# Optimization experiments

Measured on AMD Instinct MI355X. Metric: run time of the kernel, lower is better.

Reference implementation:

```python
import jax, jax.numpy as jnp
import numpy as np

DIN = 128
HID = 128
B, N = 32, 2048
NEG = 9000000000000000.0


def setup_inputs() -> dict:
    key = jax.random.key(0)
    ks = jax.random.split(key, 8)
    x = jax.random.normal(ks[0], (B, N, DIN), dtype=jnp.float32)
    mask = jax.random.randint(ks[1], (B, N, N), 0, 2).astype(jnp.float32)
    s = 1.0 / np.sqrt(DIN)
    Wv = jax.random.uniform(ks[2], (DIN, HID), minval=-s, maxval=s, dtype=jnp.float32)
    bv = jax.random.uniform(ks[3], (HID,), minval=-s, maxval=s, dtype=jnp.float32)
    Wk = jax.random.uniform(ks[4], (DIN, HID), minval=-s, maxval=s, dtype=jnp.float32)
    bk = jax.random.uniform(ks[5], (HID,), minval=-s, maxval=s, dtype=jnp.float32)
    Wq = jax.random.uniform(ks[6], (DIN, HID), minval=-s, maxval=s, dtype=jnp.float32)
    bq = jax.random.uniform(ks[7], (HID,), minval=-s, maxval=s, dtype=jnp.float32)
    return {"x": x, "mask": mask, "Wv": Wv, "bv": bv, "Wk": Wk, "bk": bk, "Wq": Wq, "bq": bq}


def reference(x, mask, Wv, bv, Wk, bk, Wq, bq):
    v = jnp.tanh(x @ Wv + bv)            # [B, N, H]
    q = jnp.tanh(x @ Wq + bq)            # [B, N, H]
    k = jnp.tanh(x @ Wk + bk)            # [B, N, H]
    scores = jnp.einsum('bih,bjh->bij', q, k)  # [B, N, N]
    scores = scores * mask - NEG * (1.0 - mask)
    att = jax.nn.softmax(scores, axis=-1)
    out = jnp.einsum('bij,bjh->bih', att, v)   # [B, N, H]
    return out
```

## Files before the change

### kernel.cpp

```cpp
#include <hip/hip_runtime.h>

#define DIN 128
#define HID 128
#define BB  32
#define NN  2048
#define LOG2E 1.44269504088896340736f

typedef float  f32x4   __attribute__((ext_vector_type(4)));
typedef __bf16 bf16x4v __attribute__((ext_vector_type(4)));
typedef __bf16 bf16x8  __attribute__((ext_vector_type(8)));

__device__ __forceinline__ float tanh_fast(float x) {
  float e = __expf(2.0f * x);
  return 1.0f - 2.0f / (e + 1.0f);
}

__global__ __launch_bounds__(256) void wt_kernel(
    const float* __restrict__ Wq, const float* __restrict__ Wk,
    const float* __restrict__ Wv, __bf16* __restrict__ wt) {
  const float* W = (blockIdx.x == 0) ? Wq : (blockIdx.x == 1) ? Wk : Wv;
  __bf16* dst = wt + blockIdx.x * (DIN * HID);
  int t = threadIdx.x;
#pragma unroll
  for (int c = 0; c < 16; ++c) {
    int o = c * 1024 + t * 4;
    int d = o >> 7, h = o & 127;
    f32x4 v = *(const f32x4*)(W + d * HID + h);
    dst[(h + 0) * DIN + d] = (__bf16)v.x;
    dst[(h + 1) * DIN + d] = (__bf16)v.y;
    dst[(h + 2) * DIN + d] = (__bf16)v.z;
    dst[(h + 3) * DIN + d] = (__bf16)v.w;
  }
}

__global__ __launch_bounds__(256) void proj_kernel(
    const float* __restrict__ x, const __bf16* __restrict__ wt,
    const float* __restrict__ bq, const float* __restrict__ bk,
    const float* __restrict__ bv, __bf16* __restrict__ qbf,
    __bf16* __restrict__ kbf, __bf16* __restrict__ vtbf) {
  int tid = threadIdx.x;
  int lane = tid & 63, w = tid >> 6;
  int l15 = lane & 15, quad = lane >> 4;
  long i0 = (long)blockIdx.x * 64;

  bf16x8 bx[4][4];
#pragma unroll
  for (int nt = 0; nt < 4; ++nt) {
    const float* xp = x + (i0 + nt * 16 + l15) * DIN;
#pragma unroll
    for (int ks = 0; ks < 4; ++ks) {
      int d0 = ks * 32 + quad * 8;
      f32x4 a = *(const f32x4*)(xp + d0);
      f32x4 b = *(const f32x4*)(xp + d0 + 4);
      bf16x8 f;
      f[0] = (__bf16)a.x; f[1] = (__bf16)a.y; f[2] = (__bf16)a.z; f[3] = (__bf16)a.w;
      f[4] = (__bf16)b.x; f[5] = (__bf16)b.y; f[6] = (__bf16)b.z; f[7] = (__bf16)b.w;
      bx[nt][ks] = f;
    }
  }

#pragma unroll
  for (int p = 0; p < 2; ++p) {
    const __bf16* wtp = wt + p * DIN * HID;
    const float* bias = (p == 0) ? bq : bk;
    __bf16* outp = (p == 0) ? qbf : kbf;
#pragma unroll
    for (int nt = 0; nt < 8; ++nt) {
      int h0 = nt * 16 + l15;
      f32x4 acc = {0.f, 0.f, 0.f, 0.f};
#pragma unroll
      for (int ks = 0; ks < 4; ++ks) {
        bf16x8 wf = *(const bf16x8*)(wtp + (long)h0 * DIN + ks * 32 + quad * 8);
        acc = __builtin_amdgcn_mfma_f32_16x16x32_bf16(bx[w][ks], wf, acc, 0, 0, 0);
      }
      float bcol = bias[h0];
      long rowb = i0 + w * 16 + quad * 4;
#pragma unroll
      for (int r = 0; r < 4; ++r) {
        float val = tanh_fast(acc[r] + bcol);
        if (p == 0) val *= LOG2E;
        outp[(rowb + r) * HID + h0] = (__bf16)val;
      }
    }
  }

  {
    const __bf16* wtp = wt + 2 * DIN * HID;
    long bb = i0 >> 11;
    int nloc = (int)(i0 & 2047);
    long vbase = bb * (long)HID * NN;
#pragma unroll
    for (int s = 0; s < 2; ++s) {
      int hb = w * 32 + s * 16;
      bf16x8 af[4];
#pragma unroll
      for (int ks = 0; ks < 4; ++ks)
        af[ks] = *(const bf16x8*)(wtp + (long)(hb + l15) * DIN + ks * 32 + quad * 8);
      float bvr[4];
#pragma unroll
      for (int r = 0; r < 4; ++r) bvr[r] = bv[hb + quad * 4 + r];
#pragma unroll
      for (int nt = 0; nt < 4; ++nt) {
        f32x4 acc = {0.f, 0.f, 0.f, 0.f};
#pragma unroll
        for (int ks = 0; ks < 4; ++ks)
          acc = __builtin_amdgcn_mfma_f32_16x16x32_bf16(af[ks], bx[nt][ks], acc, 0, 0, 0);
        int hrow = hb + quad * 4;
        int ncol = nloc + nt * 16 + l15;
#pragma unroll
        for (int r = 0; r < 4; ++r) {
          float val = tanh_fast(acc[r] + bvr[r]);
          vtbf[vbase + (long)(hrow + r) * NN + ncol] = (__bf16)val;
        }
      }
    }
  }
}

__global__ __launch_bounds__(512, 4) void attn_kernel(
    const __bf16* __restrict__ qbf, const __bf16* __restrict__ kbf,
    const __bf16* __restrict__ vtbf, const float* __restrict__ mask,
    float* __restrict__ out) {
  __shared__ __bf16 Ks[2][64 * 128];
  __shared__ __bf16 Vts[2][128 * 64];

  const int tid = threadIdx.x;
  const int lane = tid & 63, w = tid >> 6;
  const int l15 = lane & 15, quad = lane >> 4;
  const int swz = (l15 & 7) << 3;
  const int bid = blockIdx.x;
  const int vb = (bid >> 3) | ((bid & 7) << 6);
  const int b = vb >> 4;
  const int i0 = (vb & 15) * 128;
  const long kvbase = (long)b * NN * HID;

  bf16x8 qf[4];
  {
    const __bf16* qp = qbf + kvbase + (long)(i0 + w * 16 + l15) * HID + quad * 8;
#pragma unroll
    for (int ks = 0; ks < 4; ++ks) qf[ks] = *(const bf16x8*)(qp + ks * 32);
  }

  const int krl = (w << 3) + (lane >> 3);
  const int kcl = (lane & 7) * 8;
  const int vrl = (w << 4) + (lane >> 2);
  const int vcl = (lane & 3) * 8;
  const __bf16* kg = kbf + kvbase + (long)krl * HID + kcl;
  const __bf16* vg = vtbf + (long)b * HID * NN + (long)vrl * NN + vcl;
  const int ksw0 = krl * 128 + (kcl ^ ((krl & 7) << 3));
  const int ksw1 = krl * 128 + ((kcl + 64) ^ ((krl & 7) << 3));
  const int vsw0 = vrl * 64 + (vcl ^ ((vrl & 7) << 3));
  const int vsw1 = vrl * 64 + ((vcl + 32) ^ ((vrl & 7) << 3));
  const float* mp = mask + ((long)b * NN + (i0 + w * 16 + l15)) * NN + quad * 4;

  f32x4 O[8];
#pragma unroll
  for (int i = 0; i < 8; ++i) O[i] = (f32x4){0.f, 0.f, 0.f, 0.f};
  float mrow = -1e30f, lrow = 0.0f;

  bf16x8 kr0 = *(const bf16x8*)(kg);
  bf16x8 kr1 = *(const bf16x8*)(kg + 64);
  bf16x8 vr0 = *(const bf16x8*)(vg);
  bf16x8 vr1 = *(const bf16x8*)(vg + 32);
  f32x4 mr[4];
#pragma unroll
  for (int t = 0; t < 4; ++t) mr[t] = *(const f32x4*)(mp + t * 16);
  *(bf16x8*)&Ks[0][ksw0] = kr0; *(bf16x8*)&Ks[0][ksw1] = kr1;
  *(bf16x8*)&Vts[0][vsw0] = vr0; *(bf16x8*)&Vts[0][vsw1] = vr1;
  unsigned mbits;
  {
    float mb = 0.f;
#pragma unroll
    for (int t = 0; t < 4; ++t)
#pragma unroll
      for (int r = 0; r < 4; ++r)
        mb = fmaf(mr[t][r], (float)(1u << (t * 4 + r)), mb);
    mbits = (unsigned)mb;
  }
  __syncthreads();

  int cur = 0;
  for (int jt = 0; jt < 32; ++jt) {
    const int jn = (jt < 31) ? jt + 1 : 31;
    {
      const __bf16* kgn = kg + (long)jn * 64 * HID;
      kr0 = *(const bf16x8*)(kgn);
      kr1 = *(const bf16x8*)(kgn + 64);
      const __bf16* vgn = vg + jn * 64;
      vr0 = *(const bf16x8*)(vgn);
      vr1 = *(const bf16x8*)(vgn + 32);
#pragma unroll
      for (int t = 0; t < 4; ++t) mr[t] = *(const f32x4*)(mp + jn * 64 + t * 16);
    }

    f32x4 pt[4];
#pragma unroll
    for (int t = 0; t < 4; ++t) {
      f32x4 acc = {0.f, 0.f, 0.f, 0.f};
      const int krow = t * 16 + l15;
#pragma unroll
      for (int ks = 0; ks < 4; ++ks) {
        bf16x8 kf = *(const bf16x8*)&Ks[cur][krow * 128 + ((quad * 8 + ks * 32) ^ swz)];
        acc = __builtin_amdgcn_mfma_f32_16x16x32_bf16(kf, qf[ks], acc, 0, 0, 0);
      }
      pt[t] = acc;
    }

    float tmx = -1e30f;
#pragma unroll
    for (int t = 0; t < 4; ++t)
#pragma unroll
      for (int r = 0; r < 4; ++r) {
        float s = ((mbits >> (t * 4 + r)) & 1u) ? pt[t][r] : -1e30f;
        pt[t][r] = s;
        tmx = fmaxf(tmx, s);
      }
    tmx = fmaxf(tmx, __shfl_xor(tmx, 16));
    tmx = fmaxf(tmx, __shfl_xor(tmx, 32));
    const bool grow = !__all(tmx <= mrow);
    const float mnew = fmaxf(mrow, tmx);
    const float alpha = exp2f(mrow - mnew);
    float rs = 0.0f;
#pragma unroll
    for (int t = 0; t < 4; ++t)
#pragma unroll
      for (int r = 0; r < 4; ++r) {
        float p = exp2f(pt[t][r] - mnew);
        pt[t][r] = p;
        rs += p;
      }
    rs += __shfl_xor(rs, 16);
    rs += __shfl_xor(rs, 32);
    lrow = lrow * alpha + rs;
    mrow = mnew;

    if (grow) {
      float ar[4];
#pragma unroll
      for (int r = 0; r < 4; ++r) ar[r] = __shfl(alpha, (quad << 2) + r);
#pragma unroll
      for (int nt = 0; nt < 8; ++nt)
#pragma unroll
        for (int r = 0; r < 4; ++r) O[nt][r] *= ar[r];
    }

    __bf16* Pw = &Ks[cur ^ 1][w * 1024];
#pragma unroll
    for (int t = 0; t < 4; ++t) {
      bf16x4v pb;
#pragma unroll
      for (int r = 0; r < 4; ++r) pb[r] = (__bf16)pt[t][r];
      *(bf16x4v*)&Pw[l15 * 64 + ((t * 16 + quad * 4) ^ swz)] = pb;
    }
    const bf16x8 pf0 = *(const bf16x8*)&Pw[l15 * 64 + ((quad * 8) ^ swz)];
    const bf16x8 pf1 = *(const bf16x8*)&Pw[l15 * 64 + ((quad * 8 + 32) ^ swz)];

#pragma unroll
    for (int nt = 0; nt < 8; ++nt) {
      const int vrow = nt * 16 + l15;
      bf16x8 vf0 = *(const bf16x8*)&Vts[cur][vrow * 64 + ((quad * 8) ^ swz)];
      bf16x8 vf1 = *(const bf16x8*)&Vts[cur][vrow * 64 + ((quad * 8 + 32) ^ swz)];
      O[nt] = __builtin_amdgcn_mfma_f32_16x16x32_bf16(pf0, vf0, O[nt], 0, 0, 0);
      O[nt] = __builtin_amdgcn_mfma_f32_16x16x32_bf16(pf1, vf1, O[nt], 0, 0, 0);
    }

    *(bf16x8*)&Ks[cur ^ 1][ksw0] = kr0; *(bf16x8*)&Ks[cur ^ 1][ksw1] = kr1;
    *(bf16x8*)&Vts[cur ^ 1][vsw0] = vr0; *(bf16x8*)&Vts[cur ^ 1][vsw1] = vr1;
    {
      float mb = 0.f;
#pragma unroll
      for (int t = 0; t < 4; ++t)
#pragma unroll
        for (int r = 0; r < 4; ++r)
          mb = fmaf(mr[t][r], (float)(1u << (t * 4 + r)), mb);
      mbits = (unsigned)mb;
    }
    __syncthreads();
    cur ^= 1;
  }

  const float inv = 1.0f / lrow;
  float il[4];
#pragma unroll
  for (int r = 0; r < 4; ++r) il[r] = __shfl(inv, (quad << 2) + r);
  const long rowb = (long)b * NN + i0 + w * 16 + quad * 4;
#pragma unroll
  for (int r = 0; r < 4; ++r) {
    float* op = out + (rowb + r) * HID;
#pragma unroll
    for (int nt = 0; nt < 8; ++nt) op[nt * 16 + l15] = O[nt][r] * il[r];
  }
}

extern "C" void kernel_launch(void* const* d_in, const int* in_sizes, int n_in,
                              void* d_out, int out_size, void* d_ws, size_t ws_size,
                              hipStream_t stream) {
  const float* x    = (const float*)d_in[0];
  const float* mask = (const float*)d_in[1];
  const float* Wv   = (const float*)d_in[2];
  const float* bv   = (const float*)d_in[3];
  const float* Wk   = (const float*)d_in[4];
  const float* bk   = (const float*)d_in[5];
  const float* Wq   = (const float*)d_in[6];
  const float* bq   = (const float*)d_in[7];
  float* out = (float*)d_out;

  __bf16* ws = (__bf16*)d_ws;
  __bf16* wt   = ws;
  __bf16* qbf  = ws + 3 * DIN * HID;
  __bf16* kbf  = qbf + (long)BB * NN * HID;
  __bf16* vtbf = kbf + (long)BB * NN * HID;

  wt_kernel<<<3, 256, 0, stream>>>(Wq, Wk, Wv, wt);
  proj_kernel<<<BB * NN / 64, 256, 0, stream>>>(x, wt, bq, bk, bv, qbf, kbf, vtbf);
  attn_kernel<<<512, 512, 0, stream>>>(qbf, kbf, vtbf, mask, out);
}
```

Before: 893.3 us.

## Switch attention kernel to 32x32x16 MFMA with register-resident P and 4 waves

Rewrites the attention kernel to use 32x32x16 bf16 MFMAs, with each wave owning 32 query rows instead of 16 and blocks shrinking to 256 threads. Probabilities are passed to the PV MFMA through cross-half lane shuffles instead of a round trip through shared memory. The output store becomes row-contiguous float4 writes. The aim is fewer MFMA issues, fewer LDS accesses and a cheaper output store, in exchange for more accumulator registers per thread and fewer waves per block.

```diff
diff --git a/kernel.cpp b/kernel.cpp
--- a/kernel.cpp
+++ b/kernel.cpp
@@ -7,12 +7,19 @@
 #define LOG2E 1.44269504088896340736f
 
 typedef float  f32x4   __attribute__((ext_vector_type(4)));
+typedef float  f32x16  __attribute__((ext_vector_type(16)));
 typedef __bf16 bf16x4v __attribute__((ext_vector_type(4)));
 typedef __bf16 bf16x8  __attribute__((ext_vector_type(8)));
 
 __device__ __forceinline__ float tanh_fast(float x) {
   float e = __expf(2.0f * x);
   return 1.0f - 2.0f / (e + 1.0f);
+}
+
+__device__ __forceinline__ unsigned pack2bf(float x, float y) {
+  union { unsigned u; __bf16 h[2]; } t;
+  t.h[0] = (__bf16)x; t.h[1] = (__bf16)y;
+  return t.u;
 }
 
 __global__ __launch_bounds__(256) void wt_kernel(
@@ -117,7 +124,7 @@
   }
 }
 
-__global__ __launch_bounds__(512, 4) void attn_kernel(
+__global__ __launch_bounds__(256, 2) void attn_kernel(
     const __bf16* __restrict__ qbf, const __bf16* __restrict__ kbf,
     const __bf16* __restrict__ vtbf, const float* __restrict__ mask,
     float* __restrict__ out) {
@@ -126,56 +133,62 @@
 
   const int tid = threadIdx.x;
   const int lane = tid & 63, w = tid >> 6;
-  const int l15 = lane & 15, quad = lane >> 4;
-  const int swz = (l15 & 7) << 3;
+  const int l31 = lane & 31, H = lane >> 5;
+  const int swz = (l31 & 7) << 3;
   const int bid = blockIdx.x;
   const int vb = (bid >> 3) | ((bid & 7) << 6);
   const int b = vb >> 4;
   const int i0 = (vb & 15) * 128;
   const long kvbase = (long)b * NN * HID;
-
-  bf16x8 qf[4];
+  const int qrow = i0 + w * 32 + l31;
+
+  bf16x8 qf[8];
   {
-    const __bf16* qp = qbf + kvbase + (long)(i0 + w * 16 + l15) * HID + quad * 8;
-#pragma unroll
-    for (int ks = 0; ks < 4; ++ks) qf[ks] = *(const bf16x8*)(qp + ks * 32);
-  }
-
-  const int krl = (w << 3) + (lane >> 3);
-  const int kcl = (lane & 7) * 8;
-  const int vrl = (w << 4) + (lane >> 2);
-  const int vcl = (lane & 3) * 8;
-  const __bf16* kg = kbf + kvbase + (long)krl * HID + kcl;
-  const __bf16* vg = vtbf + (long)b * HID * NN + (long)vrl * NN + vcl;
-  const int ksw0 = krl * 128 + (kcl ^ ((krl & 7) << 3));
-  const int ksw1 = krl * 128 + ((kcl + 64) ^ ((krl & 7) << 3));
-  const int vsw0 = vrl * 64 + (vcl ^ ((vrl & 7) << 3));
-  const int vsw1 = vrl * 64 + ((vcl + 32) ^ ((vrl & 7) << 3));
-  const float* mp = mask + ((long)b * NN + (i0 + w * 16 + l15)) * NN + quad * 4;
-
-  f32x4 O[8];
-#pragma unroll
-  for (int i = 0; i < 8; ++i) O[i] = (f32x4){0.f, 0.f, 0.f, 0.f};
+    const __bf16* qp = qbf + kvbase + (long)qrow * HID + H * 8;
+#pragma unroll
+    for (int kd = 0; kd < 8; ++kd) qf[kd] = *(const bf16x8*)(qp + kd * 16);
+  }
+
+  const __bf16* kg = kbf + kvbase + (long)tid * 8;
+  const int ksw = (tid >> 4) * 128 + (((tid & 15) * 8) ^ (((tid >> 4) & 7) << 3));
+  const int vrow = tid >> 1, vcolb = (tid & 1) * 32;
+  const __bf16* vg = vtbf + (long)b * HID * NN + (long)vrow * NN + vcolb;
+  int vsw[4];
+#pragma unroll
+  for (int u = 0; u < 4; ++u)
+    vsw[u] = vrow * 64 + ((vcolb + u * 8) ^ ((vrow & 7) << 3));
+  const float* mp = mask + ((long)b * NN + qrow) * NN + H * 4;
+
+  f32x16 O[4];
+#pragma unroll
+  for (int ht = 0; ht < 4; ++ht)
+#pragma unroll
+    for (int r = 0; r < 16; ++r) O[ht][r] = 0.f;
   float mrow = -1e30f, lrow = 0.0f;
 
-  bf16x8 kr0 = *(const bf16x8*)(kg);
-  bf16x8 kr1 = *(const bf16x8*)(kg + 64);
-  bf16x8 vr0 = *(const bf16x8*)(vg);
-  bf16x8 vr1 = *(const bf16x8*)(vg + 32);
-  f32x4 mr[4];
-#pragma unroll
-  for (int t = 0; t < 4; ++t) mr[t] = *(const f32x4*)(mp + t * 16);
-  *(bf16x8*)&Ks[0][ksw0] = kr0; *(bf16x8*)&Ks[0][ksw1] = kr1;
-  *(bf16x8*)&Vts[0][vsw0] = vr0; *(bf16x8*)&Vts[0][vsw1] = vr1;
+  bf16x8 kr[4], vr[4];
+  f32x4 mr[8];
+#pragma unroll
+  for (int u = 0; u < 4; ++u) kr[u] = *(const bf16x8*)(kg + u * 2048);
+#pragma unroll
+  for (int u = 0; u < 4; ++u) vr[u] = *(const bf16x8*)(vg + u * 8);
+#pragma unroll
+  for (int g = 0; g < 8; ++g) mr[g] = *(const f32x4*)(mp + g * 8);
+#pragma unroll
+  for (int u = 0; u < 4; ++u) *(bf16x8*)&Ks[0][u * 2048 + ksw] = kr[u];
+#pragma unroll
+  for (int u = 0; u < 4; ++u) *(bf16x8*)&Vts[0][vsw[u]] = vr[u];
   unsigned mbits;
   {
-    float mb = 0.f;
-#pragma unroll
-    for (int t = 0; t < 4; ++t)
-#pragma unroll
-      for (int r = 0; r < 4; ++r)
-        mb = fmaf(mr[t][r], (float)(1u << (t * 4 + r)), mb);
-    mbits = (unsigned)mb;
+    float lo = 0.f, hi = 0.f;
+#pragma unroll
+    for (int g = 0; g < 4; ++g)
+#pragma unroll
+      for (int e = 0; e < 4; ++e) {
+        lo = fmaf(mr[g][e],     (float)(1u << (g * 4 + e)), lo);
+        hi = fmaf(mr[g + 4][e], (float)(1u << (g * 4 + e)), hi);
+      }
+    mbits = (unsigned)lo | ((unsigned)hi << 16);
   }
   __syncthreads();
 
@@ -183,113 +196,118 @@
   for (int jt = 0; jt < 32; ++jt) {
     const int jn = (jt < 31) ? jt + 1 : 31;
     {
-      const __bf16* kgn = kg + (long)jn * 64 * HID;
-      kr0 = *(const bf16x8*)(kgn);
-      kr1 = *(const bf16x8*)(kgn + 64);
+      const __bf16* kgn = kg + (long)jn * 8192;
+#pragma unroll
+      for (int u = 0; u < 4; ++u) kr[u] = *(const bf16x8*)(kgn + u * 2048);
       const __bf16* vgn = vg + jn * 64;
-      vr0 = *(const bf16x8*)(vgn);
-      vr1 = *(const bf16x8*)(vgn + 32);
-#pragma unroll
-      for (int t = 0; t < 4; ++t) mr[t] = *(const f32x4*)(mp + jn * 64 + t * 16);
-    }
-
-    f32x4 pt[4];
-#pragma unroll
-    for (int t = 0; t < 4; ++t) {
-      f32x4 acc = {0.f, 0.f, 0.f, 0.f};
-      const int krow = t * 16 + l15;
-#pragma unroll
-      for (int ks = 0; ks < 4; ++ks) {
-        bf16x8 kf = *(const bf16x8*)&Ks[cur][krow * 128 + ((quad * 8 + ks * 32) ^ swz)];
-        acc = __builtin_amdgcn_mfma_f32_16x16x32_bf16(kf, qf[ks], acc, 0, 0, 0);
-      }
-      pt[t] = acc;
+#pragma unroll
+      for (int u = 0; u < 4; ++u) vr[u] = *(const bf16x8*)(vgn + u * 8);
+      const float* mpn = mp + jn * 64;
+#pragma unroll
+      for (int g = 0; g < 8; ++g) mr[g] = *(const f32x4*)(mpn + g * 8);
+    }
+
+    f32x16 c0, c1;
+#pragma unroll
+    for (int r = 0; r < 16; ++r) { c0[r] = 0.f; c1[r] = 0.f; }
+#pragma unroll
+    for (int kd = 0; kd < 8; ++kd) {
+      const int col = (kd * 16 + H * 8) ^ swz;
+      bf16x8 kf0 = *(const bf16x8*)&Ks[cur][l31 * 128 + col];
+      bf16x8 kf1 = *(const bf16x8*)&Ks[cur][(32 + l31) * 128 + col];
+      c0 = __builtin_amdgcn_mfma_f32_32x32x16_bf16(kf0, qf[kd], c0, 0, 0, 0);
+      c1 = __builtin_amdgcn_mfma_f32_32x32x16_bf16(kf1, qf[kd], c1, 0, 0, 0);
     }
 
     float tmx = -1e30f;
 #pragma unroll
-    for (int t = 0; t < 4; ++t)
-#pragma unroll
-      for (int r = 0; r < 4; ++r) {
-        float s = ((mbits >> (t * 4 + r)) & 1u) ? pt[t][r] : -1e30f;
-        pt[t][r] = s;
-        tmx = fmaxf(tmx, s);
-      }
-    tmx = fmaxf(tmx, __shfl_xor(tmx, 16));
+    for (int r = 0; r < 16; ++r) {
+      float s0 = ((mbits >> r) & 1u) ? c0[r] : -1e30f;
+      float s1 = ((mbits >> (16 + r)) & 1u) ? c1[r] : -1e30f;
+      c0[r] = s0; c1[r] = s1;
+      tmx = fmaxf(tmx, fmaxf(s0, s1));
+    }
     tmx = fmaxf(tmx, __shfl_xor(tmx, 32));
     const bool grow = !__all(tmx <= mrow);
     const float mnew = fmaxf(mrow, tmx);
     const float alpha = exp2f(mrow - mnew);
     float rs = 0.0f;
 #pragma unroll
-    for (int t = 0; t < 4; ++t)
-#pragma unroll
-      for (int r = 0; r < 4; ++r) {
-        float p = exp2f(pt[t][r] - mnew);
-        pt[t][r] = p;
-        rs += p;
-      }
-    rs += __shfl_xor(rs, 16);
+    for (int r = 0; r < 16; ++r) {
+      float p0 = exp2f(c0[r] - mnew);
+      float p1 = exp2f(c1[r] - mnew);
+      c0[r] = p0; c1[r] = p1;
+      rs += p0 + p1;
+    }
     rs += __shfl_xor(rs, 32);
     lrow = lrow * alpha + rs;
     mrow = mnew;
 
     if (grow) {
-      float ar[4];
-#pragma unroll
-      for (int r = 0; r < 4; ++r) ar[r] = __shfl(alpha, (quad << 2) + r);
-#pragma unroll
-      for (int nt = 0; nt < 8; ++nt)
-#pragma unroll
-        for (int r = 0; r < 4; ++r) O[nt][r] *= ar[r];
-    }
-
-    __bf16* Pw = &Ks[cur ^ 1][w * 1024];
-#pragma unroll
-    for (int t = 0; t < 4; ++t) {
-      bf16x4v pb;
-#pragma unroll
-      for (int r = 0; r < 4; ++r) pb[r] = (__bf16)pt[t][r];
-      *(bf16x4v*)&Pw[l15 * 64 + ((t * 16 + quad * 4) ^ swz)] = pb;
-    }
-    const bf16x8 pf0 = *(const bf16x8*)&Pw[l15 * 64 + ((quad * 8) ^ swz)];
-    const bf16x8 pf1 = *(const bf16x8*)&Pw[l15 * 64 + ((quad * 8 + 32) ^ swz)];
-
-#pragma unroll
-    for (int nt = 0; nt < 8; ++nt) {
-      const int vrow = nt * 16 + l15;
-      bf16x8 vf0 = *(const bf16x8*)&Vts[cur][vrow * 64 + ((quad * 8) ^ swz)];
-      bf16x8 vf1 = *(const bf16x8*)&Vts[cur][vrow * 64 + ((quad * 8 + 32) ^ swz)];
-      O[nt] = __builtin_amdgcn_mfma_f32_16x16x32_bf16(pf0, vf0, O[nt], 0, 0, 0);
-      O[nt] = __builtin_amdgcn_mfma_f32_16x16x32_bf16(pf1, vf1, O[nt], 0, 0, 0);
-    }
-
-    *(bf16x8*)&Ks[cur ^ 1][ksw0] = kr0; *(bf16x8*)&Ks[cur ^ 1][ksw1] = kr1;
-    *(bf16x8*)&Vts[cur ^ 1][vsw0] = vr0; *(bf16x8*)&Vts[cur ^ 1][vsw1] = vr1;
+#pragma unroll
+      for (int ht = 0; ht < 4; ++ht)
+#pragma unroll
+        for (int r = 0; r < 16; ++r) O[ht][r] *= alpha;
+    }
+
+#pragma unroll
+    for (int s = 0; s < 4; ++s) {
+      const int rb = 8 * (s & 1);
+      unsigned pA0, pA1, pB0, pB1;
+      if (s < 2) {
+        pA0 = pack2bf(c0[rb + 0], c0[rb + 1]); pA1 = pack2bf(c0[rb + 2], c0[rb + 3]);
+        pB0 = pack2bf(c0[rb + 4], c0[rb + 5]); pB1 = pack2bf(c0[rb + 6], c0[rb + 7]);
+      } else {
+        pA0 = pack2bf(c1[rb + 0], c1[rb + 1]); pA1 = pack2bf(c1[rb + 2], c1[rb + 3]);
+        pB0 = pack2bf(c1[rb + 4], c1[rb + 5]); pB1 = pack2bf(c1[rb + 6], c1[rb + 7]);
+      }
+      unsigned snd0 = H ? pA0 : pB0;
+      unsigned snd1 = H ? pA1 : pB1;
+      unsigned rcv0 = __shfl_xor(snd0, 32);
+      unsigned rcv1 = __shfl_xor(snd1, 32);
+      union { unsigned u[4]; bf16x8 v; } pb;
+      pb.u[0] = H ? rcv0 : pA0;
+      pb.u[1] = H ? rcv1 : pA1;
+      pb.u[2] = H ? pB0 : rcv0;
+      pb.u[3] = H ? pB1 : rcv1;
+      const int vcol = (s * 16 + H * 8) ^ swz;
+#pragma unroll
+      for (int ht = 0; ht < 4; ++ht) {
+        bf16x8 vf = *(const bf16x8*)&Vts[cur][(ht * 32 + l31) * 64 + vcol];
+        O[ht] = __builtin_amdgcn_mfma_f32_32x32x16_bf16(vf, pb.v, O[ht], 0, 0, 0);
+      }
+    }
+
+#pragma unroll
+    for (int u = 0; u < 4; ++u) *(bf16x8*)&Ks[cur ^ 1][u * 2048 + ksw] = kr[u];
+#pragma unroll
+    for (int u = 0; u < 4; ++u) *(bf16x8*)&Vts[cur ^ 1][vsw[u]] = vr[u];
     {
-      float mb = 0.f;
-#pragma unroll
-      for (int t = 0; t < 4; ++t)
-#pragma unroll
-        for (int r = 0; r < 4; ++r)
-          mb = fmaf(mr[t][r], (float)(1u << (t * 4 + r)), mb);
-      mbits = (unsigned)mb;
+      float lo = 0.f, hi = 0.f;
+#pragma unroll
+      for (int g = 0; g < 4; ++g)
+#pragma unroll
+        for (int e = 0; e < 4; ++e) {
+          lo = fmaf(mr[g][e],     (float)(1u << (g * 4 + e)), lo);
+          hi = fmaf(mr[g + 4][e], (float)(1u << (g * 4 + e)), hi);
+        }
+      mbits = (unsigned)lo | ((unsigned)hi << 16);
     }
     __syncthreads();
     cur ^= 1;
   }
 
   const float inv = 1.0f / lrow;
-  float il[4];
-#pragma unroll
-  for (int r = 0; r < 4; ++r) il[r] = __shfl(inv, (quad << 2) + r);
-  const long rowb = (long)b * NN + i0 + w * 16 + quad * 4;
-#pragma unroll
-  for (int r = 0; r < 4; ++r) {
-    float* op = out + (rowb + r) * HID;
-#pragma unroll
-    for (int nt = 0; nt < 8; ++nt) op[nt * 16 + l15] = O[nt][r] * il[r];
-  }
+  float* op = out + ((long)b * NN + qrow) * HID;
+#pragma unroll
+  for (int ht = 0; ht < 4; ++ht)
+#pragma unroll
+    for (int r4 = 0; r4 < 4; ++r4) {
+      f32x4 v;
+#pragma unroll
+      for (int j = 0; j < 4; ++j) v[j] = O[ht][r4 * 4 + j] * inv;
+      *(f32x4*)(op + ht * 32 + r4 * 8 + H * 4) = v;
+    }
 }
 
 extern "C" void kernel_launch(void* const* d_in, const int* in_sizes, int n_in,
@@ -313,5 +331,5 @@
 
   wt_kernel<<<3, 256, 0, stream>>>(Wq, Wk, Wv, wt);
   proj_kernel<<<BB * NN / 64, 256, 0, stream>>>(x, wt, bq, bk, bv, qbf, kbf, vtbf);
-  attn_kernel<<<512, 512, 0, stream>>>(qbf, kbf, vtbf, mask, out);
-}
+  attn_kernel<<<512, 256, 0, stream>>>(qbf, kbf, vtbf, mask, out);
+}
```

Measured after the change: 874.3 us. 1.02x faster.
